# Kernel optimization log

Hardware: AMD Instinct MI355X
Metric: run time of the kernel (lower is better)

## Reference

```python
import jax, jax.numpy as jnp
import numpy as np

B, S, H = 2, 2048, 4096
NH, NKV, HD = 32, 8, 128
ROPE_THETA = 10000.0


def _rope_cos_sin():
    inv_freq = 1.0 / (ROPE_THETA ** (jnp.arange(0, HD, 2, dtype=jnp.float32) / HD))  # [HD/2]
    pos = jnp.arange(S, dtype=jnp.float32)
    freqs = pos[:, None] * inv_freq[None, :]            # [S, HD/2]
    emb = jnp.concatenate([freqs, freqs], axis=-1)      # [S, HD]
    cos = jnp.broadcast_to(jnp.cos(emb)[None], (B, S, HD))
    sin = jnp.broadcast_to(jnp.sin(emb)[None], (B, S, HD))
    return cos, sin


def setup_inputs() -> dict:
    key = jax.random.key(0)
    k0, k1, k2, k3, k4 = jax.random.split(key, 5)
    std = 0.02
    hidden_states = jax.random.normal(k0, (B, S, H), dtype=jnp.float32)
    wq = jax.random.normal(k1, (H, NH * HD), dtype=jnp.float32) * std
    wk = jax.random.normal(k2, (H, NKV * HD), dtype=jnp.float32) * std
    wv = jax.random.normal(k3, (H, NKV * HD), dtype=jnp.float32) * std
    wo = jax.random.normal(k4, (NH * HD, H), dtype=jnp.float32) * std
    cos, sin = _rope_cos_sin()
    return {"hidden_states": hidden_states, "cos": cos, "sin": sin,
            "wq": wq, "wk": wk, "wv": wv, "wo": wo}


def _rotate_half(x):
    x1, x2 = jnp.split(x, 2, axis=-1)
    return jnp.concatenate([-x2, x1], axis=-1)


def reference(hidden_states, cos, sin, wq, wk, wv, wo):
    scale = HD ** -0.5
    # QKV projections -> [B, n_heads, S, HD]
    q = (hidden_states @ wq).reshape(B, S, NH, HD).transpose(0, 2, 1, 3)
    k = (hidden_states @ wk).reshape(B, S, NKV, HD).transpose(0, 2, 1, 3)
    v = (hidden_states @ wv).reshape(B, S, NKV, HD).transpose(0, 2, 1, 3)
    # RoPE: cos/sin [B,S,HD] -> broadcast over heads (unsqueeze_dim=1)
    c = cos[:, None, :, :]
    s = sin[:, None, :, :]
    q = q * c + _rotate_half(q) * s
    k = k * c + _rotate_half(k) * s
    # GQA: repeat_interleave kv heads to match query heads
    n_rep = NH // NKV
    k = jnp.repeat(k, n_rep, axis=1)  # [B, NH, S, HD]
    v = jnp.repeat(v, n_rep, axis=1)
    # causal attention
    scores = jnp.einsum('bhqd,bhkd->bhqk', q, k) * scale  # [B,NH,S,S]
    causal = jnp.tril(jnp.ones((S, S), dtype=bool))
    scores = jnp.where(causal[None, None], scores, jnp.finfo(scores.dtype).min)
    probs = jax.nn.softmax(scores, axis=-1)
    attn = jnp.einsum('bhqk,bhkd->bhqd', probs, v)        # [B,NH,S,HD]
    attn = attn.transpose(0, 2, 1, 3).reshape(B, S, NH * HD)
    return attn @ wo
```

## Files before the change

kernel.cpp:

```cpp
#include <hip/hip_runtime.h>

#define B_ 2
#define S_ 2048
#define H_ 4096
#define NH_ 32
#define NKV_ 8
#define HD_ 128
#define QST 4096
#define KVS 2048

typedef __bf16 bf16;
typedef __bf16 bf16x8 __attribute__((ext_vector_type(8)));
typedef float floatx4 __attribute__((ext_vector_type(4)));
typedef float floatx16 __attribute__((ext_vector_type(16)));
typedef unsigned int u32;

static __device__ __forceinline__ floatx4 fzero4() {
    floatx4 v; v[0] = 0.f; v[1] = 0.f; v[2] = 0.f; v[3] = 0.f; return v;
}

static __device__ __forceinline__ void gload16(const bf16* g, bf16* l) {
    __builtin_amdgcn_global_load_lds((const __attribute__((address_space(1))) u32*)g,
                                     (__attribute__((address_space(3))) u32*)l,
                                     16, 0, 0);
}

__global__ void conv_f32_bf16(const float* __restrict__ in, bf16* __restrict__ out) {
    const long long N = (long long)4096 * 4096;
    long long i = ((long long)blockIdx.x * 256 + threadIdx.x) * 8;
    const long long stride = (long long)gridDim.x * 256 * 8;
    for (; i < N; i += stride) {
        float4 a = *(const float4*)(in + i);
        float4 b = *(const float4*)(in + i + 4);
        bf16x8 h;
        h[0] = (bf16)a.x; h[1] = (bf16)a.y; h[2] = (bf16)a.z; h[3] = (bf16)a.w;
        h[4] = (bf16)b.x; h[5] = (bf16)b.y; h[6] = (bf16)b.z; h[7] = (bf16)b.w;
        *(bf16x8*)(out + i) = h;
    }
}

template <typename TC>
__global__ __launch_bounds__(512) void gemm256(const bf16* __restrict__ A,
                                               const bf16* __restrict__ Bt0,
                                               const bf16* __restrict__ Bt1,
                                               int nsplit,
                                               TC* __restrict__ C0,
                                               TC* __restrict__ C1,
                                               int csplit,
                                               int lda, int ldC0, int ldC1) {
    __shared__ __align__(16) bf16 lds[2][2][2][8192];

    const int tid  = threadIdx.x;
    const int wid  = tid >> 6;
    const int lane = tid & 63;
    const int quad = lane >> 4;
    const int l16  = lane & 15;
    const int wr   = wid >> 2;
    const int wc   = wid & 3;

    const u32 nbx  = gridDim.x;
    const u32 flat = blockIdx.y * nbx + blockIdx.x;
    const u32 cpx  = (nbx * gridDim.y) >> 3;
    const u32 swz  = (flat & 7) * cpx + (flat >> 3);
    const int m0   = (int)(swz / nbx) * 256;
    const int n0t  = (int)(swz % nbx) * 256;

    const bf16* Bt = (n0t < nsplit) ? Bt0 + (size_t)n0t * 4096
                                    : Bt1 + (size_t)(n0t - nsplit) * 4096;

    floatx4 acc[8][4];
#pragma unroll
    for (int i = 0; i < 8; i++)
#pragma unroll
        for (int j = 0; j < 4; j++) acc[i][j] = fzero4();

    auto stageChunk = [&](int s, int k0, int c) {
        const int op   = c >> 2;
        const int half = (c >> 1) & 1;
        const int r    = (c & 1) * 64 + (tid >> 3);
        const int gs   = tid & 7;
        const int glog = gs ^ (r & 7);
        const int G    = (c & 1) * 512 + tid;
        const bf16* src = op
            ? Bt + (size_t)(half * 128 + r) * 4096 + k0 + glog * 8
            : A + (size_t)(m0 + half * 128 + r) * lda + k0 + glog * 8;
        gload16(src, &lds[s][op][half][(size_t)G * 8]);
    };

    const int NT = 4096 / 64;
#pragma unroll
    for (int c = 0; c < 8; c++) stageChunk(0, 0, c);
#pragma unroll
    for (int c = 0; c < 8; c++) stageChunk(1, 64, c);

    for (int g = 0; g < NT; ++g) {
        const int s = g & 1;
        if (g >= 1 && g + 1 < NT) {
            const int kn = (g + 1) * 64;
#pragma unroll
            for (int c = 0; c < 8; c++) stageChunk((g + 1) & 1, kn, c);
        }
        if (g + 1 < NT) asm volatile("s_waitcnt vmcnt(8)" ::: "memory");
        else            asm volatile("s_waitcnt vmcnt(0)" ::: "memory");
        __builtin_amdgcn_sched_barrier(0);
        __builtin_amdgcn_s_barrier();

#pragma unroll
        for (int p = 0; p < 4; p++) {
            const int qm = p >> 1, qn = p & 1;
            bf16x8 af[4][2], bfr[2][2];
#pragma unroll
            for (int i = 0; i < 4; i++) {
                const int r = (qm * 4 + i) * 16 + l16;
#pragma unroll
                for (int ks = 0; ks < 2; ks++)
                    af[i][ks] = *(const bf16x8*)&lds[s][0][wr]
                        [(size_t)r * 64 + ((ks * 4 + quad) ^ (r & 7)) * 8];
            }
#pragma unroll
            for (int j = 0; j < 2; j++) {
                const int rb = (wc & 1) * 64 + (qn * 2 + j) * 16 + l16;
#pragma unroll
                for (int ks = 0; ks < 2; ks++)
                    bfr[j][ks] = *(const bf16x8*)&lds[s][1][wc >> 1]
                        [(size_t)rb * 64 + ((ks * 4 + quad) ^ (rb & 7)) * 8];
            }
            __builtin_amdgcn_s_barrier();
            __builtin_amdgcn_s_setprio(1);
#pragma unroll
            for (int i = 0; i < 4; i++)
#pragma unroll
                for (int j = 0; j < 2; j++)
#pragma unroll
                    for (int ks = 0; ks < 2; ks++)
                        acc[qm * 4 + i][qn * 2 + j] =
                            __builtin_amdgcn_mfma_f32_16x16x32_bf16(
                                af[i][ks], bfr[j][ks],
                                acc[qm * 4 + i][qn * 2 + j], 0, 0, 0);
            __builtin_amdgcn_s_setprio(0);
            __builtin_amdgcn_s_barrier();
        }
    }

    TC* Cb; int ldC, cb0;
    if (n0t < csplit) { Cb = C0; ldC = ldC0; cb0 = n0t; }
    else              { Cb = C1; ldC = ldC1; cb0 = n0t - csplit; }
#pragma unroll
    for (int fa = 0; fa < 8; fa++) {
#pragma unroll
        for (int rr = 0; rr < 4; rr++) {
            const int row = m0 + wr * 128 + fa * 16 + quad * 4 + rr;
#pragma unroll
            for (int fb = 0; fb < 4; fb++) {
                const int col = cb0 + wc * 64 + fb * 16 + l16;
                Cb[(size_t)row * ldC + col] = (TC)acc[fa][fb][rr];
            }
        }
    }
}

template <typename TI, typename TO>
__global__ void transpose_b(const TI* __restrict__ in, TO* __restrict__ out,
                            long long irs, long long ors,
                            int zdiv, long long zs1, long long zs2,
                            long long ozs) {
    __shared__ TI t[32][33];
    const int z = blockIdx.z;
    const TI* ip = in + (long long)(z / zdiv) * zs1 + (long long)(z % zdiv) * zs2;
    TO* op = out + (long long)z * ozs;
    const int r0 = blockIdx.y * 32, c0 = blockIdx.x * 32;
    const int tx = threadIdx.x, ty = threadIdx.y;
#pragma unroll
    for (int i = 0; i < 4; i++)
        t[ty + i * 8][tx] = ip[(long long)(r0 + ty + i * 8) * irs + c0 + tx];
    __syncthreads();
#pragma unroll
    for (int i = 0; i < 4; i++)
        op[(long long)(c0 + ty + i * 8) * ors + r0 + tx] = (TO)t[tx][ty + i * 8];
}

__global__ void rope_q(bf16* __restrict__ q, const float* __restrict__ cosb,
                       const float* __restrict__ sinb) {
    const float QSC = 0.08838834764831845f;
    size_t idx = (size_t)blockIdx.x * 256 + threadIdx.x;
    int dp = idx & 63;
    size_t t = idx >> 6;
    int h = (int)(t % NH_);
    size_t bs = t / NH_;
    size_t base = bs * QST + (size_t)h * HD_;
    float x1 = (float)q[base + dp];
    float x2 = (float)q[base + dp + 64];
    float c1 = cosb[bs * HD_ + dp];
    float s1 = sinb[bs * HD_ + dp];
    float c2 = cosb[bs * HD_ + dp + 64];
    float s2 = sinb[bs * HD_ + dp + 64];
    q[base + dp]      = (bf16)((x1 * c1 - x2 * s1) * QSC);
    q[base + dp + 64] = (bf16)((x2 * c2 + x1 * s2) * QSC);
}

__global__ void repack_k_rope(const bf16* __restrict__ kvb, bf16* __restrict__ kout,
                              const float* __restrict__ cosb,
                              const float* __restrict__ sinb) {
    size_t idx = (size_t)blockIdx.x * 256 + threadIdx.x;
    int dp = idx & 63;
    size_t t = idx >> 6;
    int kv = (int)(t % NKV_);
    size_t bs = t / NKV_;
    int b = (int)(bs / S_);
    int s = (int)(bs % S_);
    size_t ibase = bs * KVS + (size_t)kv * HD_;
    float x1 = (float)kvb[ibase + dp];
    float x2 = (float)kvb[ibase + dp + 64];
    float c1 = cosb[bs * HD_ + dp];
    float s1 = sinb[bs * HD_ + dp];
    float c2 = cosb[bs * HD_ + dp + 64];
    float s2 = sinb[bs * HD_ + dp + 64];
    size_t obase = (((size_t)b * NKV_ + kv) * S_ + s) * HD_;
    kout[obase + dp]      = (bf16)(x1 * c1 - x2 * s1);
    kout[obase + dp + 64] = (bf16)(x2 * c2 + x1 * s2);
}

__global__ __launch_bounds__(256) void flash_fwd(const bf16* __restrict__ Q,
                                                 const bf16* __restrict__ Kp,
                                                 const bf16* __restrict__ Vt,
                                                 bf16* __restrict__ O) {
    __shared__ __align__(16) bf16 smem[32768];

    const int bh = blockIdx.y;
    const int b = bh >> 5, h = bh & 31, kv = h >> 2;
    const int tid = threadIdx.x, w = tid >> 6, lane = tid & 63;
    const int l32 = lane & 31, hlf = lane >> 5;

    const bf16* Kb = Kp + (size_t)(b * NKV_ + kv) * S_ * HD_;
    const bf16* Vb = Vt + (size_t)(b * NKV_ + kv) * (size_t)HD_ * S_;
    const bf16* Qbase = Q + (size_t)b * S_ * QST + (size_t)h * HD_;
    bf16* Obase = O + (size_t)b * S_ * QST + (size_t)h * HD_;

    auto stage = [&](int kbase, bf16* KsB, bf16* VsB) {
#pragma unroll
        for (int i = 0; i < 4; i++) {
            int G = i * 256 + tid;
            int r = G >> 4, gp = G & 15;
            int gl = gp ^ (r & 15);
            gload16(Kb + (size_t)(kbase + r) * HD_ + gl * 8, KsB + (size_t)G * 8);
        }
#pragma unroll
        for (int i = 0; i < 4; i++) {
            int G = i * 256 + tid;
            int R = G >> 4, gp = G & 15;
            int g16 = gp ^ (R & 15);
            int d = R * 2 + (g16 >> 3);
            int kg = g16 & 7;
            gload16(Vb + (size_t)d * S_ + kbase + kg * 8, VsB + (size_t)G * 8);
        }
    };

    for (int pass = 0; pass < 2; ++pass) {
        const int qb = pass ? (15 - (int)blockIdx.x) : (int)blockIdx.x;
        const int q0 = qb * 128;
        const int wqmin = q0 + w * 32;
        const int wqmax = wqmin + 31;
        const int qrow = wqmin + l32;

        const bf16* Qr = Qbase + (size_t)qrow * QST;
        bf16x8 qf[8];
#pragma unroll
        for (int ks = 0; ks < 8; ks++)
            qf[ks] = *(const bf16x8*)(Qr + ks * 16 + hlf * 8);

        floatx16 ot[4];
#pragma unroll
        for (int dt = 0; dt < 4; dt++)
#pragma unroll
            for (int r = 0; r < 16; r++) ot[dt][r] = 0.f;
        float mi = -1e30f, li = 0.f;

        if (pass) __syncthreads();
        stage(0, smem, smem + 8192);
        __syncthreads();

        auto compute = [&](int kbase, const bf16* KsB, const bf16* VsB) {
            if (kbase > wqmax) return;
            floatx16 st[2];
#pragma unroll
            for (int n = 0; n < 2; n++)
#pragma unroll
                for (int r = 0; r < 16; r++) st[n][r] = 0.f;
#pragma unroll
            for (int ks = 0; ks < 8; ks++) {
                int phys = (ks * 2 + hlf) ^ (l32 & 15);
#pragma unroll
                for (int n = 0; n < 2; n++) {
                    bf16x8 kf = *(const bf16x8*)(KsB + (size_t)(n * 32 + l32) * 128 + phys * 8);
                    st[n] = __builtin_amdgcn_mfma_f32_32x32x16_bf16(
                        kf, qf[ks], st[n], 0, 0, 0);
                }
            }
            if (kbase + 63 > wqmin) {
#pragma unroll
                for (int n = 0; n < 2; n++)
#pragma unroll
                    for (int r = 0; r < 16; r++) {
                        int key = kbase + n * 32 + (r & 3) + 8 * (r >> 2) + 4 * hlf;
                        if (key > qrow) st[n][r] = -1e30f;
                    }
            }
            float m = st[0][0];
#pragma unroll
            for (int r = 1; r < 16; r++) m = fmaxf(m, st[0][r]);
#pragma unroll
            for (int r = 0; r < 16; r++) m = fmaxf(m, st[1][r]);
            m = fmaxf(m, __shfl_xor(m, 32));
            if (!__all(m <= mi + 8.f)) {
                float mn = fmaxf(mi, m);
                float al = __expf(mi - mn);
                mi = mn;
                li *= al;
#pragma unroll
                for (int dt = 0; dt < 4; dt++)
#pragma unroll
                    for (int r = 0; r < 16; r++) ot[dt][r] *= al;
            }
            float ls = 0.f;
#pragma unroll
            for (int n = 0; n < 2; n++)
#pragma unroll
                for (int r = 0; r < 16; r++) {
                    float p = __expf(st[n][r] - mi);
                    st[n][r] = p;
                    ls += p;
                }
            ls += __shfl_xor(ls, 32);
            li += ls;

            bf16x8 pb[4];
#pragma unroll
            for (int ks2 = 0; ks2 < 4; ks2++) {
                const int n = ks2 >> 1;
                const int rb = (ks2 & 1) * 8;
                float s0 = hlf ? st[n][rb + 0] : st[n][rb + 4];
                float s1 = hlf ? st[n][rb + 1] : st[n][rb + 5];
                float s2 = hlf ? st[n][rb + 2] : st[n][rb + 6];
                float s3 = hlf ? st[n][rb + 3] : st[n][rb + 7];
                float r0 = __shfl_xor(s0, 32);
                float r1 = __shfl_xor(s1, 32);
                float r2 = __shfl_xor(s2, 32);
                float r3 = __shfl_xor(s3, 32);
                float e0, e1, e2, e3, e4, e5, e6, e7;
                if (hlf == 0) {
                    e0 = st[n][rb + 0]; e1 = st[n][rb + 1];
                    e2 = st[n][rb + 2]; e3 = st[n][rb + 3];
                    e4 = r0; e5 = r1; e6 = r2; e7 = r3;
                } else {
                    e0 = r0; e1 = r1; e2 = r2; e3 = r3;
                    e4 = st[n][rb + 4]; e5 = st[n][rb + 5];
                    e6 = st[n][rb + 6]; e7 = st[n][rb + 7];
                }
                bf16x8 t;
                t[0] = (bf16)e0; t[1] = (bf16)e1; t[2] = (bf16)e2; t[3] = (bf16)e3;
                t[4] = (bf16)e4; t[5] = (bf16)e5; t[6] = (bf16)e6; t[7] = (bf16)e7;
                pb[ks2] = t;
            }

#pragma unroll
            for (int ks2 = 0; ks2 < 4; ks2++) {
#pragma unroll
                for (int dt = 0; dt < 4; dt++) {
                    int d = dt * 32 + l32;
                    int g16 = ((d & 1) * 8 + ks2 * 2 + hlf) ^ ((d >> 1) & 15);
                    bf16x8 vf = *(const bf16x8*)(VsB + (size_t)(d >> 1) * 128 + g16 * 8);
                    ot[dt] = __builtin_amdgcn_mfma_f32_32x32x16_bf16(
                        vf, pb[ks2], ot[dt], 0, 0, 0);
                }
            }
        };

        const int nT = 2 * qb + 2;
        for (int j = 0; j < nT; j += 2) {
            stage((j + 1) * 64, smem + 16384, smem + 24576);
            compute(j * 64, smem, smem + 8192);
            __syncthreads();
            if (j + 2 < nT) stage((j + 2) * 64, smem, smem + 8192);
            compute((j + 1) * 64, smem + 16384, smem + 24576);
            __syncthreads();
        }

        {
            const float inv = 1.f / li;
            bf16* Os = smem + (size_t)w * 32 * 136;
#pragma unroll
            for (int dt = 0; dt < 4; dt++)
#pragma unroll
                for (int r = 0; r < 16; r++) {
                    int d = dt * 32 + (r & 3) + 8 * (r >> 2) + 4 * hlf;
                    Os[l32 * 136 + d] = (bf16)(ot[dt][r] * inv);
                }
        }
        __syncthreads();
        {
#pragma unroll
            for (int i = 0; i < 8; i++) {
                int u = i * 256 + tid;
                int qa = u >> 4, gr = u & 15;
                bf16x8 v = *(const bf16x8*)(smem + (size_t)qa * 136 + gr * 8);
                *(bf16x8*)(Obase + (size_t)(q0 + qa) * QST + gr * 8) = v;
            }
        }
    }
}

extern "C" void kernel_launch(void* const* d_in, const int* in_sizes, int n_in,
                              void* d_out, int out_size, void* d_ws, size_t ws_size,
                              hipStream_t stream) {
    const float* hs   = (const float*)d_in[0];
    const float* cosb = (const float*)d_in[1];
    const float* sinb = (const float*)d_in[2];
    const float* wq   = (const float*)d_in[3];
    const float* wk   = (const float*)d_in[4];
    const float* wv   = (const float*)d_in[5];
    const float* wo   = (const float*)d_in[6];
    float* out = (float*)d_out;
    (void)in_sizes; (void)n_in; (void)out_size;

    const size_t NEED = (size_t)72 * 1024 * 1024;
    if (ws_size < NEED) return;

    char* ws = (char*)d_ws;
    bf16* qbuf = (bf16*)ws;
    bf16* kvb  = (bf16*)(ws + (size_t)32 * 1024 * 1024);
    bf16* R1   = (bf16*)(ws + (size_t)48 * 1024 * 1024);
    bf16* woHi = kvb;

    bf16* hsb  = (bf16*)d_out;
    bf16* BtHi = (bf16*)((char*)d_out + (size_t)32 * 1024 * 1024);

    dim3 tb(32, 8, 1);

    conv_f32_bf16<<<2048, 256, 0, stream>>>(hs, hsb);

    transpose_b<float, bf16><<<dim3(96, 128, 1), tb, 0, stream>>>(
        wq, R1, 4096, 4096, 1, 0, 0, 0);
    transpose_b<float, bf16><<<dim3(32, 128, 1), tb, 0, stream>>>(
        wq + 3072, BtHi, 4096, 4096, 1, 0, 0, 0);
    transpose_b<float, bf16><<<dim3(32, 128, 1), tb, 0, stream>>>(
        wk, BtHi + (size_t)1024 * 4096, 1024, 4096, 1, 0, 0, 0);
    transpose_b<float, bf16><<<dim3(32, 128, 1), tb, 0, stream>>>(
        wv, BtHi + (size_t)2048 * 4096, 1024, 4096, 1, 0, 0, 0);

    gemm256<bf16><<<dim3(24, 16), 512, 0, stream>>>(
        hsb, R1, BtHi, 3072, qbuf, kvb, 4096, 4096, QST, KVS);

    rope_q<<<(B_ * S_ * NH_ * 64) / 256, 256, 0, stream>>>(qbuf, cosb, sinb);
    bf16* Kpk = R1;
    bf16* Vtv = R1 + (size_t)B_ * NKV_ * S_ * HD_;
    repack_k_rope<<<(B_ * S_ * NKV_ * 64) / 256, 256, 0, stream>>>(
        kvb, Kpk, cosb, sinb);
    transpose_b<bf16, bf16><<<dim3(HD_ / 32, S_ / 32, B_ * NKV_), tb, 0, stream>>>(
        kvb + 1024, Vtv, KVS, S_,
        NKV_, (long long)S_ * KVS, HD_, (long long)HD_ * S_);

    flash_fwd<<<dim3(8, B_ * NH_), 256, 0, stream>>>(qbuf, Kpk, Vtv, qbuf);

    transpose_b<float, bf16><<<dim3(96, 128, 1), tb, 0, stream>>>(
        wo, R1, 4096, 4096, 1, 0, 0, 0);
    transpose_b<float, bf16><<<dim3(32, 128, 1), tb, 0, stream>>>(
        wo + 3072, woHi, 4096, 4096, 1, 0, 0, 0);
    gemm256<float><<<dim3(16, 16), 512, 0, stream>>>(
        qbuf, R1, woHi, 3072, out, out, 1 << 30, QST, 4096, 4096);
}
```

Baseline: 842.1 us.

## Switch GEMM to 32x32x16 MFMA with new LDS swizzle; pipeline attention K/V loads

The projection GEMM moves from 16x16x32 MFMA tiles to 32x32x16 tiles, with a new 16-slot XOR swizzle for the LDS staging layout and a rewritten epilogue to match the new accumulator layout. This lowers the number of MFMA issues and LDS fragment reads per K step. The attention loop is restructured into a single-step double-buffered pipeline that issues the next tile's async loads before computing the current one, and waits on vmcnt counters instead of full syncthreads. MFMA sections are wrapped in setprio. The risks are LDS bank conflicts with the new swizzle and correctness of the vmcnt(8) assumption about how many loads stage issues.

```diff
diff --git a/kernel.cpp b/kernel.cpp
--- a/kernel.cpp
+++ b/kernel.cpp
@@ -14,10 +14,6 @@
 typedef float floatx4 __attribute__((ext_vector_type(4)));
 typedef float floatx16 __attribute__((ext_vector_type(16)));
 typedef unsigned int u32;
-
-static __device__ __forceinline__ floatx4 fzero4() {
-    floatx4 v; v[0] = 0.f; v[1] = 0.f; v[2] = 0.f; v[3] = 0.f; return v;
-}
 
 static __device__ __forceinline__ void gload16(const bf16* g, bf16* l) {
     __builtin_amdgcn_global_load_lds((const __attribute__((address_space(1))) u32*)g,
@@ -53,8 +49,8 @@
     const int tid  = threadIdx.x;
     const int wid  = tid >> 6;
     const int lane = tid & 63;
-    const int quad = lane >> 4;
-    const int l16  = lane & 15;
+    const int l32  = lane & 31;
+    const int hlf  = lane >> 5;
     const int wr   = wid >> 2;
     const int wc   = wid & 3;
 
@@ -68,22 +64,26 @@
     const bf16* Bt = (n0t < nsplit) ? Bt0 + (size_t)n0t * 4096
                                     : Bt1 + (size_t)(n0t - nsplit) * 4096;
 
-    floatx4 acc[8][4];
-#pragma unroll
-    for (int i = 0; i < 8; i++)
-#pragma unroll
-        for (int j = 0; j < 4; j++) acc[i][j] = fzero4();
+    floatx16 acc[4][2];
+#pragma unroll
+    for (int i = 0; i < 4; i++)
+#pragma unroll
+        for (int j = 0; j < 2; j++)
+#pragma unroll
+            for (int r = 0; r < 16; r++) acc[i][j][r] = 0.f;
 
     auto stageChunk = [&](int s, int k0, int c) {
         const int op   = c >> 2;
         const int half = (c >> 1) & 1;
-        const int r    = (c & 1) * 64 + (tid >> 3);
-        const int gs   = tid & 7;
-        const int glog = gs ^ (r & 7);
         const int G    = (c & 1) * 512 + tid;
+        const int R    = G >> 4, gp = G & 15;
+        const int g16  = gp ^ (R & 15);
+        const int rl   = R * 2 + (g16 >> 3);
+        const int kg   = g16 & 7;
+        const int row  = half * 128 + rl;
         const bf16* src = op
-            ? Bt + (size_t)(half * 128 + r) * 4096 + k0 + glog * 8
-            : A + (size_t)(m0 + half * 128 + r) * lda + k0 + glog * 8;
+            ? Bt + (size_t)row * 4096 + k0 + kg * 8
+            : A + (size_t)(m0 + row) * lda + k0 + kg * 8;
         gload16(src, &lds[s][op][half][(size_t)G * 8]);
     };
 
@@ -107,36 +107,29 @@
 
 #pragma unroll
         for (int p = 0; p < 4; p++) {
-            const int qm = p >> 1, qn = p & 1;
-            bf16x8 af[4][2], bfr[2][2];
-#pragma unroll
-            for (int i = 0; i < 4; i++) {
-                const int r = (qm * 4 + i) * 16 + l16;
-#pragma unroll
-                for (int ks = 0; ks < 2; ks++)
-                    af[i][ks] = *(const bf16x8*)&lds[s][0][wr]
-                        [(size_t)r * 64 + ((ks * 4 + quad) ^ (r & 7)) * 8];
-            }
-#pragma unroll
-            for (int j = 0; j < 2; j++) {
-                const int rb = (wc & 1) * 64 + (qn * 2 + j) * 16 + l16;
-#pragma unroll
-                for (int ks = 0; ks < 2; ks++)
-                    bfr[j][ks] = *(const bf16x8*)&lds[s][1][wc >> 1]
-                        [(size_t)rb * 64 + ((ks * 4 + quad) ^ (rb & 7)) * 8];
+            bf16x8 af[4], bfv[2];
+#pragma unroll
+            for (int fa = 0; fa < 4; fa++) {
+                const int r = wr * 128 + fa * 32 + l32;
+                const int half = r >> 7, rl = r & 127, R = rl >> 1;
+                const int slot = (((rl & 1) << 3) | (p * 2 + hlf)) ^ (R & 15);
+                af[fa] = *(const bf16x8*)&lds[s][0][half][(size_t)R * 128 + slot * 8];
+            }
+#pragma unroll
+            for (int fb = 0; fb < 2; fb++) {
+                const int r = wc * 64 + fb * 32 + l32;
+                const int half = r >> 7, rl = r & 127, R = rl >> 1;
+                const int slot = (((rl & 1) << 3) | (p * 2 + hlf)) ^ (R & 15);
+                bfv[fb] = *(const bf16x8*)&lds[s][1][half][(size_t)R * 128 + slot * 8];
             }
             __builtin_amdgcn_s_barrier();
             __builtin_amdgcn_s_setprio(1);
 #pragma unroll
-            for (int i = 0; i < 4; i++)
-#pragma unroll
-                for (int j = 0; j < 2; j++)
-#pragma unroll
-                    for (int ks = 0; ks < 2; ks++)
-                        acc[qm * 4 + i][qn * 2 + j] =
-                            __builtin_amdgcn_mfma_f32_16x16x32_bf16(
-                                af[i][ks], bfr[j][ks],
-                                acc[qm * 4 + i][qn * 2 + j], 0, 0, 0);
+            for (int fa = 0; fa < 4; fa++)
+#pragma unroll
+                for (int fb = 0; fb < 2; fb++)
+                    acc[fa][fb] = __builtin_amdgcn_mfma_f32_32x32x16_bf16(
+                        af[fa], bfv[fb], acc[fa][fb], 0, 0, 0);
             __builtin_amdgcn_s_setprio(0);
             __builtin_amdgcn_s_barrier();
         }
@@ -146,17 +139,16 @@
     if (n0t < csplit) { Cb = C0; ldC = ldC0; cb0 = n0t; }
     else              { Cb = C1; ldC = ldC1; cb0 = n0t - csplit; }
 #pragma unroll
-    for (int fa = 0; fa < 8; fa++) {
-#pragma unroll
-        for (int rr = 0; rr < 4; rr++) {
-            const int row = m0 + wr * 128 + fa * 16 + quad * 4 + rr;
-#pragma unroll
-            for (int fb = 0; fb < 4; fb++) {
-                const int col = cb0 + wc * 64 + fb * 16 + l16;
-                Cb[(size_t)row * ldC + col] = (TC)acc[fa][fb][rr];
-            }
-        }
-    }
+    for (int fa = 0; fa < 4; fa++)
+#pragma unroll
+        for (int fb = 0; fb < 2; fb++) {
+            const int col = cb0 + wc * 64 + fb * 32 + l32;
+#pragma unroll
+            for (int r = 0; r < 16; r++) {
+                const int row = m0 + wr * 128 + fa * 32 + (r & 3) + 8 * (r >> 2) + 4 * hlf;
+                Cb[(size_t)row * ldC + col] = (TC)acc[fa][fb][r];
+            }
+        }
 }
 
 template <typename TI, typename TO>
@@ -275,10 +267,6 @@
             for (int r = 0; r < 16; r++) ot[dt][r] = 0.f;
         float mi = -1e30f, li = 0.f;
 
-        if (pass) __syncthreads();
-        stage(0, smem, smem + 8192);
-        __syncthreads();
-
         auto compute = [&](int kbase, const bf16* KsB, const bf16* VsB) {
             if (kbase > wqmax) return;
             floatx16 st[2];
@@ -286,6 +274,7 @@
             for (int n = 0; n < 2; n++)
 #pragma unroll
                 for (int r = 0; r < 16; r++) st[n][r] = 0.f;
+            __builtin_amdgcn_s_setprio(1);
 #pragma unroll
             for (int ks = 0; ks < 8; ks++) {
                 int phys = (ks * 2 + hlf) ^ (l32 & 15);
@@ -296,6 +285,7 @@
                         kf, qf[ks], st[n], 0, 0, 0);
                 }
             }
+            __builtin_amdgcn_s_setprio(0);
             if (kbase + 63 > wqmin) {
 #pragma unroll
                 for (int n = 0; n < 2; n++)
@@ -362,6 +352,7 @@
                 pb[ks2] = t;
             }
 
+            __builtin_amdgcn_s_setprio(1);
 #pragma unroll
             for (int ks2 = 0; ks2 < 4; ks2++) {
 #pragma unroll
@@ -373,16 +364,28 @@
                         vf, pb[ks2], ot[dt], 0, 0, 0);
                 }
             }
+            __builtin_amdgcn_s_setprio(0);
         };
 
+        if (pass) __syncthreads();
+        stage(0, smem, smem + 8192);
+
         const int nT = 2 * qb + 2;
-        for (int j = 0; j < nT; j += 2) {
-            stage((j + 1) * 64, smem + 16384, smem + 24576);
-            compute(j * 64, smem, smem + 8192);
-            __syncthreads();
-            if (j + 2 < nT) stage((j + 2) * 64, smem, smem + 8192);
-            compute((j + 1) * 64, smem + 16384, smem + 24576);
-            __syncthreads();
+        for (int j = 0; j < nT; ++j) {
+            bf16* cur = smem + (size_t)(j & 1) * 16384;
+            if (j + 1 < nT) {
+                bf16* nxt = smem + (size_t)((j + 1) & 1) * 16384;
+                stage((j + 1) * 64, nxt, nxt + 8192);
+                asm volatile("s_waitcnt vmcnt(8)" ::: "memory");
+            } else {
+                asm volatile("s_waitcnt vmcnt(0)" ::: "memory");
+            }
+            __builtin_amdgcn_sched_barrier(0);
+            __builtin_amdgcn_s_barrier();
+            compute(j * 64, cur, cur + 8192);
+            asm volatile("s_waitcnt lgkmcnt(0)" ::: "memory");
+            __builtin_amdgcn_sched_barrier(0);
+            __builtin_amdgcn_s_barrier();
         }
 
         {
```

After: 795.5 us. 1.06x faster.
